# Performance work log

Measured on AMD Instinct MI355X. Metric: run time of the kernel, lower is better.

Reference implementation:

```python
import jax, jax.numpy as jnp
import numpy as np


def setup_inputs() -> dict:
    key = jax.random.key(0)
    k1, k2, k3, k4 = jax.random.split(key, 4)
    B = 50000    # batch nodes (len(neighbor_lists))
    E = 800000   # total neighbor edges (avg degree 16)
    N = 100000   # unique neighbor embedding rows
    D = 96       # feature dim
    embedding = jax.random.normal(k1, (B * 0 + N, D), dtype=jnp.float32)
    self_feats = jax.random.normal(k2, (B, D), dtype=jnp.float32)
    neighbor_idx = jax.random.randint(k3, (E,), 0, N, dtype=jnp.int64)
    seg_ids = jnp.sort(jax.random.randint(k4, (E,), 0, B, dtype=jnp.int64))
    return {
        "embedding": embedding,
        "self_feats": self_feats,
        "neighbor_idx": neighbor_idx,
        "seg_ids": seg_ids,
    }


def reference(embedding, self_feats, neighbor_idx, seg_ids):
    # Segment-mean aggregation: equivalent to the original's row-normalized
    # dense mask matmul mask.mm(embedding[neighbors_new_index]), but without
    # materializing the [B, n_unique] mask.
    B = self_feats.shape[0]
    gathered = embedding[neighbor_idx]                          # [E, D]
    sums = jax.ops.segment_sum(gathered, seg_ids, num_segments=B)   # [B, D]
    counts = jax.ops.segment_sum(
        jnp.ones(seg_ids.shape, dtype=embedding.dtype), seg_ids, num_segments=B
    )                                                            # [B]
    # every batch node has >=1 neighbor in the original; guard div-by-zero
    feats_1 = sums / jnp.maximum(counts, 1)[:, None]             # neighbor mean
    feats_2 = self_feats - feats_1
    return jnp.concatenate([feats_1, feats_2], axis=1)          # [B, 2D]
```

## Files before the change

kernel.cpp:

```cpp
#include <hip/hip_runtime.h>
#include <stdint.h>

#define DIMS 96
#define VEC 4
#define LANES (DIMS / VEC)
#define SEGS_PER_BLOCK 8
#define THREADS (LANES * SEGS_PER_BLOCK)
#define UNROLL 8

typedef float vfloat4 __attribute__((ext_vector_type(4)));


__global__ __launch_bounds__(THREADS) void seg_mean_concat_kernel(
    const float* __restrict__ emb,
    const float* __restrict__ self_feats,
    const int*   __restrict__ nidx,
    const int*   __restrict__ seg,
    float* __restrict__ out,
    int B, int E)
{
    __shared__ int sb[SEGS_PER_BLOCK + 1];

    const int b0  = blockIdx.x * SEGS_PER_BLOCK;
    const int tid = threadIdx.x;

    if (tid <= SEGS_PER_BLOCK) {
        const int v = b0 + tid;
        int lo = 0, hi = E;
        while (lo < hi) {
            const int mid = (lo + hi) >> 1;
            if (seg[mid] < v) lo = mid + 1; else hi = mid;
        }
        sb[tid] = lo;
    }
    __syncthreads();

    const int g    = tid / LANES;
    const int lane = tid - g * LANES;
    const int b    = b0 + g;
    if (b >= B) return;

    const int start = sb[g];
    const int end   = sb[g + 1];

    const vfloat4* __restrict__ embv = (const vfloat4*)emb;

    const vfloat4* sfp = (const vfloat4*)(self_feats + (size_t)b * DIMS + lane * VEC);
    const vfloat4 sf = __builtin_nontemporal_load(sfp);

    vfloat4 a0 = (vfloat4)(0.f);
    vfloat4 a1 = (vfloat4)(0.f);

    const int last = end - 1;
    if (start <= last) {
        int j[UNROLL];
#pragma unroll
        for (int k = 0; k < UNROLL; ++k) {
            int ee = start + k;
            ee = ee > last ? last : ee;
            j[k] = __builtin_nontemporal_load(nidx + ee);
        }
        __builtin_amdgcn_sched_group_barrier(0x20 , UNROLL, 0);

        for (int e = start; e <= last; e += UNROLL) {
            vfloat4 v[UNROLL];
#pragma unroll
            for (int k = 0; k < UNROLL; ++k)
                v[k] = embv[(size_t)j[k] * LANES + lane];
            __builtin_amdgcn_sched_group_barrier(0x20 , UNROLL, 0);

            const int en = e + UNROLL;
            if (en <= last) {
#pragma unroll
                for (int k = 0; k < UNROLL; ++k) {
                    int ee = en + k;
                    ee = ee > last ? last : ee;
                    j[k] = __builtin_nontemporal_load(nidx + ee);
                }
                __builtin_amdgcn_sched_group_barrier(0x20 , UNROLL, 0);
            }

#pragma unroll
            for (int k = 0; k < UNROLL; k += 2) {
                const float w0 = (e + k     <= last) ? 1.0f : 0.0f;
                const float w1 = (e + k + 1 <= last) ? 1.0f : 0.0f;
                a0 += v[k] * w0;
                a1 += v[k + 1] * w1;
            }
        }
    }

    const int cnt = end - start;
    const float inv = 1.0f / (float)(cnt > 0 ? cnt : 1);
    const vfloat4 mean = (a0 + a1) * inv;
    const vfloat4 diff = sf - mean;

    float* orow = out + (size_t)b * (2 * DIMS);
    __builtin_nontemporal_store(mean, (vfloat4*)(orow + lane * VEC));
    __builtin_nontemporal_store(diff, (vfloat4*)(orow + DIMS + lane * VEC));
}

extern "C" void kernel_launch(void* const* d_in, const int* in_sizes, int n_in,
                              void* d_out, int out_size, void* d_ws, size_t ws_size,
                              hipStream_t stream) {
    const float* emb        = (const float*)d_in[0];
    const float* self_feats = (const float*)d_in[1];
    const int*   nidx       = (const int*)d_in[2];
    const int*   seg        = (const int*)d_in[3];
    float*       out        = (float*)d_out;

    const int B = in_sizes[1] / DIMS;
    const int E = in_sizes[2];

    const int grid = (B + SEGS_PER_BLOCK - 1) / SEGS_PER_BLOCK;
    hipLaunchKernelGGL(seg_mean_concat_kernel, dim3(grid), dim3(THREADS), 0, stream,
                       emb, self_feats, nidx, seg, out, B, E);
}
```

Baseline: 63.04 us.

## Replace per-thread binary searches with wave-parallel search and boundary scan

The nine per-thread binary searches over the sorted segment array are replaced by a single 64-way wave-cooperative search using ballot/popcount to find the block's first edge. Segment boundaries are then found by having all threads scan consecutive seg entries and write boundary positions to shared memory, looping until the last boundary is filled. This cuts the serial chain of dependent global loads in the prologue at the cost of extra barriers, a scan loop, and more code complexity.

```diff
diff --git a/kernel.cpp b/kernel.cpp
--- a/kernel.cpp
+++ b/kernel.cpp
@@ -1,5 +1,6 @@
 #include <hip/hip_runtime.h>
 #include <stdint.h>
+#include <limits.h>
 
 #define DIMS 96
 #define VEC 4
@@ -20,20 +21,58 @@
     int B, int E)
 {
     __shared__ int sb[SEGS_PER_BLOCK + 1];
+    __shared__ int s_start0;
 
     const int b0  = blockIdx.x * SEGS_PER_BLOCK;
     const int tid = threadIdx.x;
+    const int bhi = b0 + SEGS_PER_BLOCK;
 
-    if (tid <= SEGS_PER_BLOCK) {
-        const int v = b0 + tid;
+    if (tid >= 1 && tid <= SEGS_PER_BLOCK) sb[tid] = -1;
+
+    if (tid < 64) {
         int lo = 0, hi = E;
-        while (lo < hi) {
-            const int mid = (lo + hi) >> 1;
-            if (seg[mid] < v) lo = mid + 1; else hi = mid;
+        while (hi - lo > 63) {
+            const int step = (hi - lo) >> 6;
+            const int p    = lo + tid * step;
+            const bool pred = seg[p] < b0;
+            const unsigned long long m = __ballot(pred);
+            const int c = (int)__popcll(m);
+            if (c == 0) { hi = lo; break; }
+            const int nlo = lo + (c - 1) * step + 1;
+            hi = (c < 64) ? (lo + c * step) : hi;
+            lo = nlo;
         }
-        sb[tid] = lo;
+        {
+            const int w = hi - lo;
+            const bool pred = (tid < w) && (seg[lo + tid] < b0);
+            const unsigned long long m = __ballot(pred);
+            lo += (int)__popcll(m);
+        }
+        if (tid == 0) { s_start0 = lo; sb[0] = lo; }
     }
     __syncthreads();
+
+    const int start0 = s_start0;
+
+    for (int r = 0; ; ++r) {
+        const int pos = start0 + r * THREADS + tid;
+        if (pos < E) {
+            const int cur  = seg[pos];
+            const int nxtv = (pos + 1 < E) ? seg[pos + 1] : INT_MAX;
+            if (r == 0 && tid == 0) {
+                const int th0 = cur < bhi ? cur : bhi;
+                for (int t = b0 + 1; t <= th0; ++t) sb[t - b0] = start0;
+            }
+            int tlo = cur + 1; if (tlo < b0 + 1) tlo = b0 + 1;
+            int thi = nxtv < bhi ? nxtv : bhi;
+            for (int t = tlo; t <= thi; ++t) sb[t - b0] = pos + 1;
+        } else if (r == 0 && tid == 0 && start0 >= E) {
+            for (int t = 1; t <= SEGS_PER_BLOCK; ++t) sb[t] = E;
+        }
+        __syncthreads();
+        if (sb[SEGS_PER_BLOCK] != -1) break;
+        __syncthreads();
+    }
 
     const int g    = tid / LANES;
     const int lane = tid - g * LANES;
```

New measurement: 56.73 us (median of 2 runs). 10.0% less time.
